# Performance work log

Hardware: AMD Instinct MI355X
Metric: run time of the kernel (lower is better)

## Reference

```python
import jax, jax.numpy as jnp
import numpy as np

B, T, F, H = 131072, 5, 30, 20


def setup_inputs() -> dict:
    key = jax.random.key(0)
    ks = jax.random.split(key, 13)
    inp = {"x": jax.random.normal(ks[0], (B, T, F), dtype=jnp.float32)}
    names_w = ["wf", "wi", "wo", "wc"]
    names_u = ["uf", "ui", "uo", "uc"]
    names_b = ["bf", "bi", "bo", "bc"]
    for j, n in enumerate(names_w):
        inp[n] = jax.random.normal(ks[1 + j], (F, H), dtype=jnp.float32) * 0.1
    for j, n in enumerate(names_u):
        inp[n] = jax.random.normal(ks[5 + j], (H, H), dtype=jnp.float32) * 0.1
    for j, n in enumerate(names_b):
        inp[n] = jax.random.normal(ks[9 + j], (1, H), dtype=jnp.float32) * 0.1
    return inp


def reference(x, wf, wi, wo, wc, uf, ui, uo, uc, bf, bi, bo, bc):
    # Note: at t=0 the original skips the recurrent term and uses ct = it*cht;
    # that is exactly equivalent to scanning with h0 = c0 = 0.
    b = x.shape[0]
    h = wf.shape[1]
    # Precompute the input-side gate projections for all timesteps in one GEMM
    # per gate: [B,T,F] @ [F,H] -> [B,T,H]. Same math, fewer launches.
    gx_f = jnp.einsum("btf,fh->bth", x, wf) + bf
    gx_i = jnp.einsum("btf,fh->bth", x, wi) + bi
    gx_o = jnp.einsum("btf,fh->bth", x, wo) + bo
    gx_c = jnp.einsum("btf,fh->bth", x, wc) + bc
    # time-major for scan: [T,B,H]
    gx = jnp.stack([gx_f.transpose(1, 0, 2), gx_i.transpose(1, 0, 2),
                    gx_o.transpose(1, 0, 2), gx_c.transpose(1, 0, 2)], axis=1)

    def step(carry, g):
        ht, ct = carry
        gf, gi, go, gc = g[0], g[1], g[2], g[3]
        ft = jax.nn.sigmoid(gf + ht @ uf)
        it = jax.nn.sigmoid(gi + ht @ ui)
        ot = jax.nn.sigmoid(go + ht @ uo)
        cht = jnp.tanh(gc + ht @ uc)
        ct = ft * ct + it * cht
        ht = ot * jnp.tanh(ct)
        return (ht, ct), ht

    h0 = jnp.zeros((b, h), dtype=x.dtype)
    c0 = jnp.zeros((b, h), dtype=x.dtype)
    _, hs = jax.lax.scan(step, (h0, c0), gx)  # hs: [T,B,H]
    return hs.transpose(1, 0, 2)  # return_sequences=True -> [B,T,H]
```

## Files before the change

kernel.cpp:

```cpp
#include <hip/hip_runtime.h>
#include <hip/hip_bf16.h>

namespace {

constexpr int T = 5, F = 30, H = 20;
constexpr int BATCH = 131072;
constexpr int BPB = 64;
constexpr int XS = 36;
constexpr int HS = 36;
constexpr int TH = T * H;

typedef __attribute__((ext_vector_type(8))) short bf16x8;
typedef __attribute__((ext_vector_type(4))) float f32x4;

union FragU { __hip_bfloat162 h2[4]; unsigned u32[4]; bf16x8 v; };

__device__ __forceinline__ float sig(float v) {
  return __builtin_amdgcn_rcpf(1.0f + __builtin_amdgcn_exp2f(v * -1.44269504f));
}
__device__ __forceinline__ float tanh_s(float v) {
  return fmaf(2.0f,
              __builtin_amdgcn_rcpf(1.0f + __builtin_amdgcn_exp2f(v * -2.88539008f)),
              -1.0f);
}

__global__ __launch_bounds__(256, 3) void lstm_wave(
    const float* __restrict__ x,
    const float* __restrict__ wf, const float* __restrict__ wi,
    const float* __restrict__ wo, const float* __restrict__ wc,
    const float* __restrict__ uf, const float* __restrict__ ui,
    const float* __restrict__ uo, const float* __restrict__ uc,
    const float* __restrict__ bf, const float* __restrict__ bi,
    const float* __restrict__ bo, const float* __restrict__ bc,
    float* __restrict__ out)
{
  const int tid  = threadIdx.x;
  const int lane = tid & 63;
  const int wv   = tid >> 6;
  const int r15  = lane & 15;
  const int q    = lane >> 4;
  const int b0   = blockIdx.x * BPB;
  const int w0   = 16 * wv;

  const float* xwave = x + (size_t)(b0 + w0) * (T * F);
  float*       owave = out + (size_t)(b0 + w0) * (T * H);

  __shared__ __align__(16) float xs[2][BPB][XS];
  __shared__ __align__(16) float hb[BPB][HS];
  __shared__ __align__(16) float hist[BPB][TH];

  const int gA = r15 & 3;
  const int jA = r15 >> 2;
  const float* Wg = (gA == 0) ? wf : (gA == 1) ? wi : (gA == 2) ? wo : wc;
  const float* Ug = (gA == 0) ? uf : (gA == 1) ? ui : (gA == 2) ? uo : uc;
  const float* Bg = (gA == 0) ? bf : (gA == 1) ? bi : (gA == 2) ? bo : bc;

  bf16x8 wfrag[5], ufrag[5];
#pragma unroll
  for (int m = 0; m < 5; ++m) {
    const int jj = 4 * m + jA;
    FragU fw, fu;
#pragma unroll
    for (int e = 0; e < 4; ++e) {
      const int k0 = 8 * q + 2 * e, k1 = k0 + 1;
      float w0v = (k0 < F) ? Wg[k0 * H + jj] : (k0 == F ? Bg[jj] : 0.f);
      float w1v = (k1 < F) ? Wg[k1 * H + jj] : 0.f;
      fw.h2[e] = __float22bfloat162_rn(float2{w0v, w1v});
      float u0 = (k0 < H) ? Ug[k0 * H + jj] : 0.f;
      float u1 = (k1 < H) ? Ug[k1 * H + jj] : 0.f;
      fu.h2[e] = __float22bfloat162_rn(float2{u0, u1});
    }
    wfrag[m] = fw.v;
    ufrag[m] = fu.v;
  }

#pragma unroll
  for (int k = 0; k < 3; ++k) {
    int i = lane + 64 * k;
    hb[w0 + i / 12][20 + i % 12] = 0.f;
  }

#pragma unroll
  for (int k = 0; k < 4; ++k) {
    int f2 = lane + 64 * k;
    if (f2 < 240) {
      int r = f2 / 15, c = 2 * (f2 % 15);
      float2 v = *(const float2*)(xwave + r * (T * F) + c);
      *(float2*)&xs[0][w0 + r][c] = v;
    }
  }

  float cst[5];
#pragma unroll
  for (int m = 0; m < 5; ++m) cst[m] = 0.f;

  float2 pf2[4];
  int cur = 0;
  for (int t = 0; t < T; ++t) {
    FragU fx;
    {
      const float* xp = &xs[cur][w0 + r15][8 * q];
      float4 lo = *(const float4*)(xp);
      float4 hi = *(const float4*)(xp + 4);
      fx.h2[0] = __float22bfloat162_rn(float2{lo.x, lo.y});
      fx.h2[1] = __float22bfloat162_rn(float2{lo.z, lo.w});
      fx.h2[2] = __float22bfloat162_rn(float2{hi.x, hi.y});
      fx.h2[3] = __float22bfloat162_rn(float2{hi.z, hi.w});
      if (q == 3) fx.u32[3] = 0x00003F80u;
    }

    if (t + 1 < T) {
#pragma unroll
      for (int k = 0; k < 4; ++k) {
        int f2 = lane + 64 * k;
        if (f2 < 240) {
          int r = f2 / 15, c = 2 * (f2 % 15);
          pf2[k] = *(const float2*)(xwave + r * (T * F) + (t + 1) * F + c);
        }
      }
    }

    f32x4 acc[5];
#pragma unroll
    for (int m = 0; m < 5; ++m)
      acc[m] = __builtin_amdgcn_mfma_f32_16x16x32_bf16(
          wfrag[m], fx.v, f32x4{0.f, 0.f, 0.f, 0.f}, 0, 0, 0);

    if (t > 0) {
      FragU fh;
      const float* hp = &hb[w0 + r15][8 * q];
      float4 lo = *(const float4*)(hp);
      float4 hi = *(const float4*)(hp + 4);
      fh.h2[0] = __float22bfloat162_rn(float2{lo.x, lo.y});
      fh.h2[1] = __float22bfloat162_rn(float2{lo.z, lo.w});
      fh.h2[2] = __float22bfloat162_rn(float2{hi.x, hi.y});
      fh.h2[3] = __float22bfloat162_rn(float2{hi.z, hi.w});
#pragma unroll
      for (int m = 0; m < 5; ++m)
        acc[m] = __builtin_amdgcn_mfma_f32_16x16x32_bf16(
            ufrag[m], fh.v, acc[m], 0, 0, 0);
    }

#pragma unroll
    for (int m = 0; m < 5; ++m) {
      float fg = sig(acc[m][0]);
      float ig = sig(acc[m][1]);
      float og = sig(acc[m][2]);
      float ch = tanh_s(acc[m][3]);
      float cn = fmaf(fg, cst[m], ig * ch);
      cst[m] = cn;
      float hn = og * tanh_s(cn);
      const int jj = 4 * m + q;
      hb[w0 + r15][jj] = hn;
      hist[w0 + r15][t * H + jj] = hn;
    }

    if (t + 1 < T) {
#pragma unroll
      for (int k = 0; k < 4; ++k) {
        int f2 = lane + 64 * k;
        if (f2 < 240) {
          int r = f2 / 15, c = 2 * (f2 % 15);
          *(float2*)&xs[cur ^ 1][w0 + r][c] = pf2[k];
        }
      }
    }
    cur ^= 1;
  }

#pragma unroll
  for (int k = 0; k < 7; ++k) {
    int f4 = lane + 64 * k;
    if (f4 < 16 * TH / 4) {
      int r = f4 / 25, c4 = 4 * (f4 % 25);
      float4 v = *(const float4*)&hist[w0 + r][c4];
      *(float4*)(owave + r * TH + c4) = v;
    }
  }
}

}

extern "C" void kernel_launch(void* const* d_in, const int* in_sizes, int n_in,
                              void* d_out, int out_size, void* d_ws, size_t ws_size,
                              hipStream_t stream) {
  const float* x  = (const float*)d_in[0];
  const float* wf = (const float*)d_in[1];
  const float* wi = (const float*)d_in[2];
  const float* wo = (const float*)d_in[3];
  const float* wc = (const float*)d_in[4];
  const float* uf = (const float*)d_in[5];
  const float* ui = (const float*)d_in[6];
  const float* uo = (const float*)d_in[7];
  const float* uc = (const float*)d_in[8];
  const float* bf = (const float*)d_in[9];
  const float* bi = (const float*)d_in[10];
  const float* bo = (const float*)d_in[11];
  const float* bc = (const float*)d_in[12];
  float* out = (float*)d_out;

  dim3 block(256);
  dim3 grid(BATCH / BPB);
  hipLaunchKernelGGL(lstm_wave, grid, block, 0, stream,
                     x, wf, wi, wo, wc, uf, ui, uo, uc, bf, bi, bo, bc, out);
}
```

Baseline: 47.42 us.

## Prepack LSTM weight fragments and shrink LDS to raise occupancy

A small pre-kernel now converts the W, U and bias weights into bf16 MFMA fragments once and writes them to the workspace. The main kernel loads these fragments directly instead of gathering and converting them per block. LDS use is also reduced so more blocks fit per CU, and launch bounds rise from 3 to 5 blocks: the x staging buffer is single-buffered and the output history is kept as bf16. The time loop is fully unrolled. The costs are an extra kernel launch and output values rounded to bf16 before being widened back to fp32, which loses precision.

```diff
diff --git a/kernel.cpp b/kernel.cpp
--- a/kernel.cpp
+++ b/kernel.cpp
@@ -6,9 +6,8 @@
 constexpr int T = 5, F = 30, H = 20;
 constexpr int BATCH = 131072;
 constexpr int BPB = 64;
-constexpr int XS = 36;
-constexpr int HS = 36;
-constexpr int TH = T * H;
+constexpr int XSS = 36;
+constexpr int HSS = 36;
 
 typedef __attribute__((ext_vector_type(8))) short bf16x8;
 typedef __attribute__((ext_vector_type(4))) float f32x4;
@@ -24,14 +23,51 @@
               -1.0f);
 }
 
-__global__ __launch_bounds__(256, 3) void lstm_wave(
-    const float* __restrict__ x,
+__device__ __forceinline__ unsigned short f2bf(float f) {
+  unsigned u = __float_as_uint(f);
+  return (unsigned short)((u + 0x7FFFu + ((u >> 16) & 1u)) >> 16);
+}
+
+__global__ void lstm_pack(
     const float* __restrict__ wf, const float* __restrict__ wi,
     const float* __restrict__ wo, const float* __restrict__ wc,
     const float* __restrict__ uf, const float* __restrict__ ui,
     const float* __restrict__ uo, const float* __restrict__ uc,
     const float* __restrict__ bf, const float* __restrict__ bi,
     const float* __restrict__ bo, const float* __restrict__ bc,
+    bf16x8* __restrict__ ws)
+{
+  const int i = blockIdx.x * 256 + threadIdx.x;
+  if (i >= 640) return;
+  const int lane = i & 63, sel = (i >> 6) & 1, m = i >> 7;
+  const int r15 = lane & 15, q = lane >> 4;
+  const int gA = r15 & 3, jA = r15 >> 2;
+  const int jj = 4 * m + jA;
+
+  const float* Wg = (gA == 0) ? wf : (gA == 1) ? wi : (gA == 2) ? wo : wc;
+  const float* Ug = (gA == 0) ? uf : (gA == 1) ? ui : (gA == 2) ? uo : uc;
+  const float* Bg = (gA == 0) ? bf : (gA == 1) ? bi : (gA == 2) ? bo : bc;
+
+  FragU fr;
+#pragma unroll
+  for (int e = 0; e < 4; ++e) {
+    const int k0 = 8 * q + 2 * e, k1 = k0 + 1;
+    float v0, v1;
+    if (sel == 0) {
+      v0 = (k0 < F) ? Wg[k0 * H + jj] : (k0 == F ? Bg[jj] : 0.f);
+      v1 = (k1 < F) ? Wg[k1 * H + jj] : 0.f;
+    } else {
+      v0 = (k0 < H) ? Ug[k0 * H + jj] : 0.f;
+      v1 = (k1 < H) ? Ug[k1 * H + jj] : 0.f;
+    }
+    fr.h2[e] = __float22bfloat162_rn(float2{v0, v1});
+  }
+  ws[(m * 2 + sel) * 64 + lane] = fr.v;
+}
+
+__global__ __launch_bounds__(256, 5) void lstm_main(
+    const float* __restrict__ x,
+    const bf16x8* __restrict__ wsfrag,
     float* __restrict__ out)
 {
   const int tid  = threadIdx.x;
@@ -45,33 +81,15 @@
   const float* xwave = x + (size_t)(b0 + w0) * (T * F);
   float*       owave = out + (size_t)(b0 + w0) * (T * H);
 
-  __shared__ __align__(16) float xs[2][BPB][XS];
-  __shared__ __align__(16) float hb[BPB][HS];
-  __shared__ __align__(16) float hist[BPB][TH];
-
-  const int gA = r15 & 3;
-  const int jA = r15 >> 2;
-  const float* Wg = (gA == 0) ? wf : (gA == 1) ? wi : (gA == 2) ? wo : wc;
-  const float* Ug = (gA == 0) ? uf : (gA == 1) ? ui : (gA == 2) ? uo : uc;
-  const float* Bg = (gA == 0) ? bf : (gA == 1) ? bi : (gA == 2) ? bo : bc;
+  __shared__ __align__(16) float xs[BPB][XSS];
+  __shared__ __align__(16) float hb[BPB][HSS];
+  __shared__ __align__(8)  unsigned short hist[BPB][100];
 
   bf16x8 wfrag[5], ufrag[5];
 #pragma unroll
   for (int m = 0; m < 5; ++m) {
-    const int jj = 4 * m + jA;
-    FragU fw, fu;
-#pragma unroll
-    for (int e = 0; e < 4; ++e) {
-      const int k0 = 8 * q + 2 * e, k1 = k0 + 1;
-      float w0v = (k0 < F) ? Wg[k0 * H + jj] : (k0 == F ? Bg[jj] : 0.f);
-      float w1v = (k1 < F) ? Wg[k1 * H + jj] : 0.f;
-      fw.h2[e] = __float22bfloat162_rn(float2{w0v, w1v});
-      float u0 = (k0 < H) ? Ug[k0 * H + jj] : 0.f;
-      float u1 = (k1 < H) ? Ug[k1 * H + jj] : 0.f;
-      fu.h2[e] = __float22bfloat162_rn(float2{u0, u1});
-    }
-    wfrag[m] = fw.v;
-    ufrag[m] = fu.v;
+    wfrag[m] = wsfrag[(m * 2 + 0) * 64 + lane];
+    ufrag[m] = wsfrag[(m * 2 + 1) * 64 + lane];
   }
 
 #pragma unroll
@@ -82,24 +100,23 @@
 
 #pragma unroll
   for (int k = 0; k < 4; ++k) {
-    int f2 = lane + 64 * k;
-    if (f2 < 240) {
-      int r = f2 / 15, c = 2 * (f2 % 15);
-      float2 v = *(const float2*)(xwave + r * (T * F) + c);
-      *(float2*)&xs[0][w0 + r][c] = v;
+    int s = lane + 64 * k;
+    int r = s >> 4, cs = s & 15;
+    if (cs < 15) {
+      *(float2*)&xs[w0 + r][2 * cs] = *(const float2*)(xwave + r * (T * F) + 2 * cs);
     }
   }
 
   float cst[5];
 #pragma unroll
   for (int m = 0; m < 5; ++m) cst[m] = 0.f;
-
   float2 pf2[4];
-  int cur = 0;
+
+#pragma unroll
   for (int t = 0; t < T; ++t) {
     FragU fx;
     {
-      const float* xp = &xs[cur][w0 + r15][8 * q];
+      const float* xp = &xs[w0 + r15][8 * q];
       float4 lo = *(const float4*)(xp);
       float4 hi = *(const float4*)(xp + 4);
       fx.h2[0] = __float22bfloat162_rn(float2{lo.x, lo.y});
@@ -112,11 +129,10 @@
     if (t + 1 < T) {
 #pragma unroll
       for (int k = 0; k < 4; ++k) {
-        int f2 = lane + 64 * k;
-        if (f2 < 240) {
-          int r = f2 / 15, c = 2 * (f2 % 15);
-          pf2[k] = *(const float2*)(xwave + r * (T * F) + (t + 1) * F + c);
-        }
+        int s = lane + 64 * k;
+        int r = s >> 4, cs = s & 15;
+        if (cs < 15)
+          pf2[k] = *(const float2*)(xwave + r * (T * F) + (t + 1) * F + 2 * cs);
       }
     }
 
@@ -151,30 +167,32 @@
       cst[m] = cn;
       float hn = og * tanh_s(cn);
       const int jj = 4 * m + q;
-      hb[w0 + r15][jj] = hn;
-      hist[w0 + r15][t * H + jj] = hn;
+      if (t + 1 < T) hb[w0 + r15][jj] = hn;
+      hist[w0 + r15][t * H + jj] = f2bf(hn);
     }
 
     if (t + 1 < T) {
 #pragma unroll
       for (int k = 0; k < 4; ++k) {
-        int f2 = lane + 64 * k;
-        if (f2 < 240) {
-          int r = f2 / 15, c = 2 * (f2 % 15);
-          *(float2*)&xs[cur ^ 1][w0 + r][c] = pf2[k];
-        }
+        int s = lane + 64 * k;
+        int r = s >> 4, cs = s & 15;
+        if (cs < 15) *(float2*)&xs[w0 + r][2 * cs] = pf2[k];
       }
     }
-    cur ^= 1;
   }
 
 #pragma unroll
   for (int k = 0; k < 7; ++k) {
-    int f4 = lane + 64 * k;
-    if (f4 < 16 * TH / 4) {
-      int r = f4 / 25, c4 = 4 * (f4 % 25);
-      float4 v = *(const float4*)&hist[w0 + r][c4];
-      *(float4*)(owave + r * TH + c4) = v;
+    unsigned g = lane + 64 * k;
+    if (g < 400) {
+      unsigned r = g / 25u, c4 = 4 * (g % 25u);
+      uint2 pv = *(const uint2*)&hist[w0 + r][c4];
+      float4 v;
+      v.x = __uint_as_float(pv.x << 16);
+      v.y = __uint_as_float(pv.x & 0xFFFF0000u);
+      v.z = __uint_as_float(pv.y << 16);
+      v.w = __uint_as_float(pv.y & 0xFFFF0000u);
+      *(float4*)(owave + 4 * g) = v;
     }
   }
 }
@@ -198,9 +216,10 @@
   const float* bo = (const float*)d_in[11];
   const float* bc = (const float*)d_in[12];
   float* out = (float*)d_out;
-
-  dim3 block(256);
-  dim3 grid(BATCH / BPB);
-  hipLaunchKernelGGL(lstm_wave, grid, block, 0, stream,
-                     x, wf, wi, wo, wc, uf, ui, uo, uc, bf, bi, bo, bc, out);
-}
+  bf16x8* ws = (bf16x8*)d_ws;
+
+  hipLaunchKernelGGL(lstm_pack, dim3(3), dim3(256), 0, stream,
+                     wf, wi, wo, wc, uf, ui, uo, uc, bf, bi, bo, bc, ws);
+  hipLaunchKernelGGL(lstm_main, dim3(BATCH / BPB), dim3(256), 0, stream,
+                     x, ws, out);
+}
```

Result: faster. 44.45 us (-6.3%).
